# Optimization experiments

Hardware: AMD Instinct MI355X
Metric: run time of the kernel (lower is better)

Reference implementation:

```python
import jax, jax.numpy as jnp
import numpy as np

IN_DIM, HIDDEN_DIM, OUT_DIM = 128, 64, 64
N_NODES, N_EDGES = 100000, 1000000


def gcn_layer(x, src, dst, W, b):
    """PyG GCNConv: h = W x; out = D^-1/2 (A+I) D^-1/2 h + b (self-loops already in src/dst)."""
    n = x.shape[0]
    deg = jax.ops.segment_sum(jnp.ones_like(src, dtype=x.dtype), dst, num_segments=n)
    dinv = jnp.where(deg > 0, jax.lax.rsqrt(deg), 0.0)
    norm = dinv[src] * dinv[dst]          # [E+N]
    h = x @ W                              # [N, out]
    msg = h[src] * norm[:, None]           # [E+N, out] gather + scale
    out = jax.ops.segment_sum(msg, dst, num_segments=n)  # scatter-add
    return out + b


def setup_inputs() -> dict:
    key = jax.random.key(0)
    k1, k2, k3, k4 = jax.random.split(key, 4)
    x = jax.random.normal(k1, (N_NODES, IN_DIM), dtype=jnp.float32)
    edge_index = jax.random.randint(k2, (2, N_EDGES), 0, N_NODES, dtype=jnp.int64)
    # Glorot-ish init for the two GCNConv linear weights; zero biases (PyG default)
    W1 = jax.random.normal(k3, (IN_DIM, HIDDEN_DIM), dtype=jnp.float32) / np.sqrt(IN_DIM)
    W2 = jax.random.normal(k4, (HIDDEN_DIM, OUT_DIM), dtype=jnp.float32) / np.sqrt(HIDDEN_DIM)
    b1 = jnp.zeros((HIDDEN_DIM,), dtype=jnp.float32)
    b2 = jnp.zeros((OUT_DIM,), dtype=jnp.float32)
    return {"x": x, "edge_index": edge_index, "W1": W1, "b1": b1, "W2": W2, "b2": b2}


def reference(x, edge_index, W1, b1, W2, b2):
    n = x.shape[0]
    loops = jnp.arange(n, dtype=edge_index.dtype)
    src = jnp.concatenate([edge_index[0], loops])  # add self-loops once
    dst = jnp.concatenate([edge_index[1], loops])
    x1 = gcn_layer(x, src, dst, W1, b1)
    h = jax.nn.relu(x1)
    # dropout is identity in eval/reference mode
    x2 = gcn_layer(h, src, dst, W2, b2)
    return x2
```

## Files before the change

kernel.cpp:

```cpp
#include <hip/hip_runtime.h>
#include <hip/hip_fp16.h>

#define DIM_IN 128
#define DIM_HID 64
#define BK_SHIFT 9
#define BK_SIZE 512
#define SRC_BITS 17
#define CAP 6144
#define CAP2 8192
#define P_EPT  16
#define P_TILE 4096

typedef _Float16 half8 __attribute__((ext_vector_type(8)));
typedef float floatx4 __attribute__((ext_vector_type(4)));


__global__ void zero_kernel(int* __restrict__ bcur, float* __restrict__ dinv_sent) {
    bcur[threadIdx.x] = 0;
    if (threadIdx.x == 0) dinv_sent[0] = 0.0f;
}


__global__ __launch_bounds__(256)
void gemm1_partition_kernel(const float* __restrict__ x, const float* __restrict__ W,
                            _Float16* __restrict__ h, int n, int gb,
                            const int* __restrict__ src, const int* __restrict__ dst,
                            int* __restrict__ bcur, int* __restrict__ part, int E) {
    __shared__ int smem[5888];
    const int tid = threadIdx.x;

    if (blockIdx.x < gb) {
        constexpr int K = DIM_IN, LDK = K + 8;
        _Float16* Wt = (_Float16*)smem;
        for (int idx = tid; idx < K * 64; idx += 256) {
            int k = idx >> 6, c = idx & 63;
            Wt[c * LDK + k] = (_Float16)W[idx];
        }
        __syncthreads();

        const int wave = tid >> 6;
        const int lane = tid & 63;
        const int r    = lane & 15;
        const int g    = lane >> 4;
        const int row0 = blockIdx.x * 64 + wave * 16;
        const int arow = row0 + r;
        const float* xrow = x + (size_t)(arow < n ? arow : 0) * K + g * 8;

        floatx4 acc0 = {}, acc1 = {}, acc2 = {}, acc3 = {};
#pragma unroll
        for (int kt = 0; kt < K / 32; ++kt) {
            float4 a0 = *(const float4*)(xrow + kt * 32);
            float4 a1 = *(const float4*)(xrow + kt * 32 + 4);
            half8 a;
            a[0] = (_Float16)a0.x; a[1] = (_Float16)a0.y;
            a[2] = (_Float16)a0.z; a[3] = (_Float16)a0.w;
            a[4] = (_Float16)a1.x; a[5] = (_Float16)a1.y;
            a[6] = (_Float16)a1.z; a[7] = (_Float16)a1.w;

            const _Float16* wb = &Wt[r * LDK + kt * 32 + g * 8];
            half8 b0 = *(const half8*)(wb + 0 * 16 * LDK);
            half8 b1 = *(const half8*)(wb + 1 * 16 * LDK);
            half8 b2 = *(const half8*)(wb + 2 * 16 * LDK);
            half8 b3 = *(const half8*)(wb + 3 * 16 * LDK);
            acc0 = __builtin_amdgcn_mfma_f32_16x16x32_f16(a, b0, acc0, 0, 0, 0);
            acc1 = __builtin_amdgcn_mfma_f32_16x16x32_f16(a, b1, acc1, 0, 0, 0);
            acc2 = __builtin_amdgcn_mfma_f32_16x16x32_f16(a, b2, acc2, 0, 0, 0);
            acc3 = __builtin_amdgcn_mfma_f32_16x16x32_f16(a, b3, acc3, 0, 0, 0);
        }

#pragma unroll
        for (int j = 0; j < 4; ++j) {
            int drow = row0 + g * 4 + j;
            _Float16* o = h + (size_t)drow * 64 + r;
            if (drow < n) {
                o[0]  = (_Float16)acc0[j];
                o[16] = (_Float16)acc1[j];
                o[32] = (_Float16)acc2[j];
                o[48] = (_Float16)acc3[j];
            } else {
                o[0] = (_Float16)0; o[16] = (_Float16)0;
                o[32] = (_Float16)0; o[48] = (_Float16)0;
            }
        }
    } else {
        int* hist  = smem;
        int* bofs  = smem + 256;
        int* gbase = smem + 512;
        int* stage = smem + 768;
        unsigned char* auxb = (unsigned char*)(smem + 4864);
        const int tile0 = (blockIdx.x - gb) * P_TILE;
        const int tcnt  = min(P_TILE, E - tile0);

        hist[tid] = 0;
        __syncthreads();

        int pack[P_EPT], bb[P_EPT], lo[P_EPT];
#pragma unroll
        for (int i = 0; i < P_EPT; ++i) {
            int e = tile0 + i * 256 + tid;
            bb[i] = -1;
            if (e < E) {
                int d = dst[e];
                int s = src[e];
                bb[i]   = d >> BK_SHIFT;
                pack[i] = ((d & (BK_SIZE - 1)) << SRC_BITS) | s;
                lo[i]   = atomicAdd(&hist[bb[i]], 1);
            }
        }
        __syncthreads();

        bofs[tid] = hist[tid];
        __syncthreads();
        for (int off = 1; off < 256; off <<= 1) {
            int t = (tid >= off) ? bofs[tid - off] : 0;
            __syncthreads();
            bofs[tid] += t;
            __syncthreads();
        }
        int ex = bofs[tid] - hist[tid];
        __syncthreads();
        bofs[tid] = ex;
        if (hist[tid]) gbase[tid] = tid * CAP + atomicAdd(&bcur[tid], hist[tid]);
        __syncthreads();

#pragma unroll
        for (int i = 0; i < P_EPT; ++i) {
            if (bb[i] >= 0) {
                int p = bofs[bb[i]] + lo[i];
                stage[p] = pack[i];
                auxb[p]  = (unsigned char)bb[i];
            }
        }
        __syncthreads();

        for (int k = tid; k < tcnt; k += 256) {
            int b = auxb[k];
            part[gbase[b] + (k - bofs[b])] = stage[k];
        }
    }
}


__global__ __launch_bounds__(256)
void bucket_fill_kernel(const int* __restrict__ bcur, const int* __restrict__ part,
                        int2* __restrict__ nodeinfo, float* __restrict__ dinv,
                        int* __restrict__ srcs, int n, int zrow) {
    __shared__ int cnt[BK_SIZE];
    __shared__ int rp[BK_SIZE];
    __shared__ int s2[256];
    __shared__ int total;
    const int tid   = threadIdx.x;
    const int bid   = blockIdx.x;
    const int node0 = bid << BK_SHIFT;
    const int bs    = min(BK_SIZE, n - node0);
    const int pbase = bid * CAP;
    const int sbase = bid * CAP2;
    const int ecnt  = bcur[bid];

    cnt[tid] = 0; cnt[tid + 256] = 0;
    __syncthreads();
    for (int k = tid; k < ecnt; k += 256)
        atomicAdd(&cnt[part[pbase + k] >> SRC_BITS], 1);
    __syncthreads();

    int c0 = cnt[2 * tid], c1 = cnt[2 * tid + 1];
    int p0 = (c0 + 3) & ~3, p1 = (c1 + 3) & ~3;
    s2[tid] = p0 + p1;
    __syncthreads();
    for (int off = 1; off < 256; off <<= 1) {
        int t = (tid >= off) ? s2[tid - off] : 0;
        __syncthreads();
        s2[tid] += t;
        __syncthreads();
    }
    int ex = s2[tid] - (p0 + p1);
    rp[2 * tid]     = ex;
    rp[2 * tid + 1] = ex + p0;
    if (tid == 255) total = s2[255];
    __syncthreads();

    for (int i = tid; i < bs; i += 256) {
        int c = cnt[i];
        nodeinfo[node0 + i] = make_int2(sbase + rp[i], (c + 3) & ~3);
        dinv[node0 + i]     = rsqrtf((float)c + 1.0f);
    }
    __syncthreads();

    cnt[tid] = 0; cnt[tid + 256] = 0;
    __syncthreads();
    for (int k = tid; k < total; k += 256) srcs[sbase + k] = zrow;
    __syncthreads();
    for (int k = tid; k < ecnt; k += 256) {
        int v    = part[pbase + k];
        int li   = v >> SRC_BITS;
        int slot = atomicAdd(&cnt[li], 1);
        srcs[sbase + rp[li] + slot] = v & ((1 << SRC_BITS) - 1);
    }
}


__global__ __launch_bounds__(256)
void layer2_fused_kernel(const int2* __restrict__ nodeinfo, const int* __restrict__ srcs,
                         const float* __restrict__ dinv, const half8* __restrict__ hs,
                         const float* __restrict__ b1, const float* __restrict__ W2,
                         _Float16* __restrict__ h2, int n) {
    __shared__ _Float16 At[64 * 72];
    __shared__ _Float16 Wt[64 * 72];
    const int tid = threadIdx.x;

    for (int idx = tid; idx < 64 * 64; idx += 256) {
        int k = idx >> 6, c = idx & 63;
        Wt[c * 72 + k] = (_Float16)W2[idx];
    }

    const int f    = tid & 7;
    const int grp  = tid >> 3;
    const int row0 = blockIdx.x * 64;

#pragma unroll
    for (int rnd = 0; rnd < 2; ++rnd) {
        const int nrow = rnd * 32 + grp;
        const int node = row0 + nrow;
        half8 o = {};
        if (node < n) {
            int2 info = nodeinfo[node];
            int start = info.x, cpad = info.y;
            float dn = dinv[node];
            half8 sv = hs[(size_t)node * 8 + f];
            float acc[8];
#pragma unroll
            for (int i = 0; i < 8; ++i) acc[i] = dn * (float)sv[i];

            if (cpad > 0) {
                int4 ss = *(const int4*)&srcs[start];
                for (int j = 0; j < cpad; j += 4) {
                    int4 nxt = *(const int4*)&srcs[start + j + 4];
                    float d0 = dinv[ss.x], d1 = dinv[ss.y], d2 = dinv[ss.z], d3 = dinv[ss.w];
                    half8 v0 = hs[(size_t)ss.x * 8 + f];
                    half8 v1 = hs[(size_t)ss.y * 8 + f];
                    half8 v2 = hs[(size_t)ss.z * 8 + f];
                    half8 v3 = hs[(size_t)ss.w * 8 + f];
#pragma unroll
                    for (int i = 0; i < 8; ++i)
                        acc[i] += (d0 * (float)v0[i] + d1 * (float)v1[i]) +
                                  (d2 * (float)v2[i] + d3 * (float)v3[i]);
                    ss = nxt;
                }
            }
#pragma unroll
            for (int i = 0; i < 8; ++i) {
                float g1 = fmaf(acc[i], dn, b1[f * 8 + i]);
                o[i] = (_Float16)fmaxf(g1, 0.0f);
            }
        }
        *(half8*)&At[nrow * 72 + f * 8] = o;
    }
    __syncthreads();

    const int wave = tid >> 6;
    const int lane = tid & 63;
    const int r    = lane & 15;
    const int g    = lane >> 4;

    floatx4 acc0 = {}, acc1 = {}, acc2 = {}, acc3 = {};
#pragma unroll
    for (int kt = 0; kt < 2; ++kt) {
        half8 a = *(const half8*)&At[(wave * 16 + r) * 72 + kt * 32 + g * 8];
        const _Float16* wb = &Wt[r * 72 + kt * 32 + g * 8];
        half8 b0 = *(const half8*)(wb + 0 * 16 * 72);
        half8 b1v = *(const half8*)(wb + 1 * 16 * 72);
        half8 b2v = *(const half8*)(wb + 2 * 16 * 72);
        half8 b3v = *(const half8*)(wb + 3 * 16 * 72);
        acc0 = __builtin_amdgcn_mfma_f32_16x16x32_f16(a, b0, acc0, 0, 0, 0);
        acc1 = __builtin_amdgcn_mfma_f32_16x16x32_f16(a, b1v, acc1, 0, 0, 0);
        acc2 = __builtin_amdgcn_mfma_f32_16x16x32_f16(a, b2v, acc2, 0, 0, 0);
        acc3 = __builtin_amdgcn_mfma_f32_16x16x32_f16(a, b3v, acc3, 0, 0, 0);
    }

#pragma unroll
    for (int j = 0; j < 4; ++j) {
        int drow = row0 + wave * 16 + g * 4 + j;
        float dn2 = (drow < n) ? dinv[drow] : 0.0f;
        _Float16* o = h2 + (size_t)drow * 64 + r;
        o[0]  = (_Float16)(acc0[j] * dn2);
        o[16] = (_Float16)(acc1[j] * dn2);
        o[32] = (_Float16)(acc2[j] * dn2);
        o[48] = (_Float16)(acc3[j] * dn2);
    }
}


__global__ __launch_bounds__(256)
void gather_out_kernel(const int2* __restrict__ nodeinfo, const int* __restrict__ srcs,
                       const float* __restrict__ dinv, const half8* __restrict__ hs,
                       const float* __restrict__ b, float* __restrict__ out, int n) {
    const int tid  = threadIdx.x;
    const int f    = tid & 7;
    const int node = blockIdx.x * 32 + (tid >> 3);
    if (node >= n) return;

    int2 info = nodeinfo[node];
    int start = info.x, cpad = info.y;

    half8 sv = hs[(size_t)node * 8 + f];
    float acc[8];
#pragma unroll
    for (int i = 0; i < 8; ++i) acc[i] = (float)sv[i];

    if (cpad > 0) {
        int4 ss = *(const int4*)&srcs[start];
        for (int j = 0; j < cpad; j += 4) {
            int4 nxt = *(const int4*)&srcs[start + j + 4];
            half8 v0 = hs[(size_t)ss.x * 8 + f];
            half8 v1 = hs[(size_t)ss.y * 8 + f];
            half8 v2 = hs[(size_t)ss.z * 8 + f];
            half8 v3 = hs[(size_t)ss.w * 8 + f];
#pragma unroll
            for (int i = 0; i < 8; ++i)
                acc[i] += ((float)v0[i] + (float)v1[i]) + ((float)v2[i] + (float)v3[i]);
            ss = nxt;
        }
    }

    float dn = dinv[node];
    const float4* b4 = (const float4*)b;
    float4 bb0 = b4[f * 2], bb1 = b4[f * 2 + 1];
    float4 o0 = make_float4(fmaf(acc[0], dn, bb0.x), fmaf(acc[1], dn, bb0.y),
                            fmaf(acc[2], dn, bb0.z), fmaf(acc[3], dn, bb0.w));
    float4 o1 = make_float4(fmaf(acc[4], dn, bb1.x), fmaf(acc[5], dn, bb1.y),
                            fmaf(acc[6], dn, bb1.z), fmaf(acc[7], dn, bb1.w));
    float4* o4 = (float4*)out;
    o4[(size_t)node * 16 + f * 2]     = o0;
    o4[(size_t)node * 16 + f * 2 + 1] = o1;
}


extern "C" void kernel_launch(void* const* d_in, const int* in_sizes, int n_in,
                              void* d_out, int out_size, void* d_ws, size_t ws_size,
                              hipStream_t stream) {
    const float* x   = (const float*)d_in[0];
    const int*   ei  = (const int*)d_in[1];
    const float* W1  = (const float*)d_in[2];
    const float* b1  = (const float*)d_in[3];
    const float* W2  = (const float*)d_in[4];
    const float* b2  = (const float*)d_in[5];
    float*       out = (float*)d_out;

    const int n = in_sizes[0] / DIM_IN;
    const int E = in_sizes[1] / 2;
    const int* srcp = ei;
    const int* dstp = ei + E;
    const int NB    = (n + BK_SIZE - 1) >> BK_SHIFT;
    const int gb    = (n + 63) / 64;
    const int pb    = (E + P_TILE - 1) / P_TILE;
    const int ab    = (n + 31) / 32;
    const size_t nrows = (size_t)gb * 64;

    const int npad = ((n + 255) / 256) * 256;

    int*      bcur     = (int*)d_ws;
    int2*     nodeinfo = (int2*)(bcur + 256);
    float*    dinv     = (float*)((int*)nodeinfo + 2 * npad);
    int*      srcs     = (int*)(dinv + npad);
    int*      part     = srcs + (size_t)NB * CAP2;
    _Float16* h        = (_Float16*)(part + (size_t)NB * CAP);
    _Float16* h2       = h + nrows * 64;

    zero_kernel<<<1, 256, 0, stream>>>(bcur, &dinv[n]);
    gemm1_partition_kernel<<<gb + pb, 256, 0, stream>>>(x, W1, h, n, gb,
                                                        srcp, dstp, bcur, part, E);
    bucket_fill_kernel<<<NB, 256, 0, stream>>>(bcur, part, nodeinfo, dinv, srcs, n, n);
    layer2_fused_kernel<<<gb, 256, 0, stream>>>(nodeinfo, srcs, dinv, (const half8*)h,
                                                b1, W2, h2, n);
    gather_out_kernel<<<ab, 256, 0, stream>>>(nodeinfo, srcs, dinv, (const half8*)h2,
                                              b2, out, n);
}
```

Baseline: 102.1 us.

## Co-schedule GEMM1 with bucket fill instead of partition, halve partition tile

Moves the layer-1 GEMM out of the partition launch and into the bucket-fill launch, so the GEMM blocks run alongside the few (~196) bucket-fill blocks instead of alongside the many partition blocks. This is meant to fill otherwise idle CUs during bucket fill. The partition tile shrinks from 4096 to 2048 edges per block, giving more blocks and less shared memory per block. The full-region zero-row fill is replaced by padding only each node's tail slots, cutting redundant stores.

```diff
diff --git a/kernel.cpp b/kernel.cpp
--- a/kernel.cpp
+++ b/kernel.cpp
@@ -8,8 +8,8 @@
 #define SRC_BITS 17
 #define CAP 6144
 #define CAP2 8192
-#define P_EPT  16
-#define P_TILE 4096
+#define P_EPT  8
+#define P_TILE 2048
 
 typedef _Float16 half8 __attribute__((ext_vector_type(8)));
 typedef float floatx4 __attribute__((ext_vector_type(4)));
@@ -22,14 +22,129 @@
 
 
 __global__ __launch_bounds__(256)
-void gemm1_partition_kernel(const float* __restrict__ x, const float* __restrict__ W,
-                            _Float16* __restrict__ h, int n, int gb,
-                            const int* __restrict__ src, const int* __restrict__ dst,
-                            int* __restrict__ bcur, int* __restrict__ part, int E) {
-    __shared__ int smem[5888];
+void partition_kernel(const int* __restrict__ src, const int* __restrict__ dst,
+                      int* __restrict__ bcur, int* __restrict__ part, int E) {
+    __shared__ int hist[256];
+    __shared__ int bofs[256];
+    __shared__ int gbase[256];
+    __shared__ int stage[P_TILE];
+    __shared__ unsigned char auxb[P_TILE];
+    const int tid   = threadIdx.x;
+    const int tile0 = blockIdx.x * P_TILE;
+    const int tcnt  = min(P_TILE, E - tile0);
+
+    hist[tid] = 0;
+    __syncthreads();
+
+    int pack[P_EPT], bb[P_EPT], lo[P_EPT];
+#pragma unroll
+    for (int i = 0; i < P_EPT; ++i) {
+        int e = tile0 + i * 256 + tid;
+        bb[i] = -1;
+        if (e < E) {
+            int d = dst[e];
+            int s = src[e];
+            bb[i]   = d >> BK_SHIFT;
+            pack[i] = ((d & (BK_SIZE - 1)) << SRC_BITS) | s;
+            lo[i]   = atomicAdd(&hist[bb[i]], 1);
+        }
+    }
+    __syncthreads();
+
+    bofs[tid] = hist[tid];
+    __syncthreads();
+    for (int off = 1; off < 256; off <<= 1) {
+        int t = (tid >= off) ? bofs[tid - off] : 0;
+        __syncthreads();
+        bofs[tid] += t;
+        __syncthreads();
+    }
+    int ex = bofs[tid] - hist[tid];
+    __syncthreads();
+    bofs[tid] = ex;
+    if (hist[tid]) gbase[tid] = tid * CAP + atomicAdd(&bcur[tid], hist[tid]);
+    __syncthreads();
+
+#pragma unroll
+    for (int i = 0; i < P_EPT; ++i) {
+        if (bb[i] >= 0) {
+            int p = bofs[bb[i]] + lo[i];
+            stage[p] = pack[i];
+            auxb[p]  = (unsigned char)bb[i];
+        }
+    }
+    __syncthreads();
+
+    for (int k = tid; k < tcnt; k += 256) {
+        int b = auxb[k];
+        part[gbase[b] + (k - bofs[b])] = stage[k];
+    }
+}
+
+
+__global__ __launch_bounds__(256)
+void fill_gemm1_kernel(const int* __restrict__ bcur, const int* __restrict__ part,
+                       int2* __restrict__ nodeinfo, float* __restrict__ dinv,
+                       int* __restrict__ srcs, int n, int NB,
+                       const float* __restrict__ x, const float* __restrict__ W,
+                       _Float16* __restrict__ h) {
+    __shared__ int smem[4352];
     const int tid = threadIdx.x;
 
-    if (blockIdx.x < gb) {
+    if (blockIdx.x < (unsigned)NB) {
+        int* cnt = smem;
+        int* rp  = smem + 512;
+        int* s2  = smem + 1024;
+        const int bid   = blockIdx.x;
+        const int node0 = bid << BK_SHIFT;
+        const int bs    = min(BK_SIZE, n - node0);
+        const int pbase = bid * CAP;
+        const int sbase = bid * CAP2;
+        const int ecnt  = bcur[bid];
+
+        cnt[tid] = 0; cnt[tid + 256] = 0;
+        __syncthreads();
+        for (int k = tid; k < ecnt; k += 256)
+            atomicAdd(&cnt[part[pbase + k] >> SRC_BITS], 1);
+        __syncthreads();
+
+        int c0 = cnt[2 * tid], c1 = cnt[2 * tid + 1];
+        int p0 = (c0 + 3) & ~3, p1 = (c1 + 3) & ~3;
+        s2[tid] = p0 + p1;
+        __syncthreads();
+        for (int off = 1; off < 256; off <<= 1) {
+            int t = (tid >= off) ? s2[tid - off] : 0;
+            __syncthreads();
+            s2[tid] += t;
+            __syncthreads();
+        }
+        int ex = s2[tid] - (p0 + p1);
+        rp[2 * tid]     = ex;
+        rp[2 * tid + 1] = ex + p0;
+        __syncthreads();
+
+        for (int i = tid; i < bs; i += 256) {
+            int c = cnt[i];
+            nodeinfo[node0 + i] = make_int2(sbase + rp[i], (c + 3) & ~3);
+            dinv[node0 + i]     = rsqrtf((float)c + 1.0f);
+        }
+        __syncthreads();
+
+        cnt[tid] = 0; cnt[tid + 256] = 0;
+        __syncthreads();
+        for (int k = tid; k < ecnt; k += 256) {
+            int v    = part[pbase + k];
+            int li   = v >> SRC_BITS;
+            int slot = atomicAdd(&cnt[li], 1);
+            srcs[sbase + rp[li] + slot] = v & ((1 << SRC_BITS) - 1);
+        }
+        __syncthreads();
+        for (int i = tid; i < bs; i += 256) {
+            int c = cnt[i];
+            int cp = (c + 3) & ~3;
+            for (int k = c; k < cp; ++k) srcs[sbase + rp[i] + k] = n;
+        }
+    } else {
         constexpr int K = DIM_IN, LDK = K + 8;
         _Float16* Wt = (_Float16*)smem;
         for (int idx = tid; idx < K * 64; idx += 256) {
@@ -42,7 +157,7 @@
         const int lane = tid & 63;
         const int r    = lane & 15;
         const int g    = lane >> 4;
-        const int row0 = blockIdx.x * 64 + wave * 16;
+        const int row0 = (blockIdx.x - NB) * 64 + wave * 16;
         const int arow = row0 + r;
         const float* xrow = x + (size_t)(arow < n ? arow : 0) * K + g * 8;
 
@@ -82,119 +197,6 @@
                 o[32] = (_Float16)0; o[48] = (_Float16)0;
             }
         }
-    } else {
-        int* hist  = smem;
-        int* bofs  = smem + 256;
-        int* gbase = smem + 512;
-        int* stage = smem + 768;
-        unsigned char* auxb = (unsigned char*)(smem + 4864);
-        const int tile0 = (blockIdx.x - gb) * P_TILE;
-        const int tcnt  = min(P_TILE, E - tile0);
-
-        hist[tid] = 0;
-        __syncthreads();
-
-        int pack[P_EPT], bb[P_EPT], lo[P_EPT];
-#pragma unroll
-        for (int i = 0; i < P_EPT; ++i) {
-            int e = tile0 + i * 256 + tid;
-            bb[i] = -1;
-            if (e < E) {
-                int d = dst[e];
-                int s = src[e];
-                bb[i]   = d >> BK_SHIFT;
-                pack[i] = ((d & (BK_SIZE - 1)) << SRC_BITS) | s;
-                lo[i]   = atomicAdd(&hist[bb[i]], 1);
-            }
-        }
-        __syncthreads();
-
-        bofs[tid] = hist[tid];
-        __syncthreads();
-        for (int off = 1; off < 256; off <<= 1) {
-            int t = (tid >= off) ? bofs[tid - off] : 0;
-            __syncthreads();
-            bofs[tid] += t;
-            __syncthreads();
-        }
-        int ex = bofs[tid] - hist[tid];
-        __syncthreads();
-        bofs[tid] = ex;
-        if (hist[tid]) gbase[tid] = tid * CAP + atomicAdd(&bcur[tid], hist[tid]);
-        __syncthreads();
-
-#pragma unroll
-        for (int i = 0; i < P_EPT; ++i) {
-            if (bb[i] >= 0) {
-                int p = bofs[bb[i]] + lo[i];
-                stage[p] = pack[i];
-                auxb[p]  = (unsigned char)bb[i];
-            }
-        }
-        __syncthreads();
-
-        for (int k = tid; k < tcnt; k += 256) {
-            int b = auxb[k];
-            part[gbase[b] + (k - bofs[b])] = stage[k];
-        }
-    }
-}
-
-
-__global__ __launch_bounds__(256)
-void bucket_fill_kernel(const int* __restrict__ bcur, const int* __restrict__ part,
-                        int2* __restrict__ nodeinfo, float* __restrict__ dinv,
-                        int* __restrict__ srcs, int n, int zrow) {
-    __shared__ int cnt[BK_SIZE];
-    __shared__ int rp[BK_SIZE];
-    __shared__ int s2[256];
-    __shared__ int total;
-    const int tid   = threadIdx.x;
-    const int bid   = blockIdx.x;
-    const int node0 = bid << BK_SHIFT;
-    const int bs    = min(BK_SIZE, n - node0);
-    const int pbase = bid * CAP;
-    const int sbase = bid * CAP2;
-    const int ecnt  = bcur[bid];
-
-    cnt[tid] = 0; cnt[tid + 256] = 0;
-    __syncthreads();
-    for (int k = tid; k < ecnt; k += 256)
-        atomicAdd(&cnt[part[pbase + k] >> SRC_BITS], 1);
-    __syncthreads();
-
-    int c0 = cnt[2 * tid], c1 = cnt[2 * tid + 1];
-    int p0 = (c0 + 3) & ~3, p1 = (c1 + 3) & ~3;
-    s2[tid] = p0 + p1;
-    __syncthreads();
-    for (int off = 1; off < 256; off <<= 1) {
-        int t = (tid >= off) ? s2[tid - off] : 0;
-        __syncthreads();
-        s2[tid] += t;
-        __syncthreads();
-    }
-    int ex = s2[tid] - (p0 + p1);
-    rp[2 * tid]     = ex;
-    rp[2 * tid + 1] = ex + p0;
-    if (tid == 255) total = s2[255];
-    __syncthreads();
-
-    for (int i = tid; i < bs; i += 256) {
-        int c = cnt[i];
-        nodeinfo[node0 + i] = make_int2(sbase + rp[i], (c + 3) & ~3);
-        dinv[node0 + i]     = rsqrtf((float)c + 1.0f);
-    }
-    __syncthreads();
-
-    cnt[tid] = 0; cnt[tid + 256] = 0;
-    __syncthreads();
-    for (int k = tid; k < total; k += 256) srcs[sbase + k] = zrow;
-    __syncthreads();
-    for (int k = tid; k < ecnt; k += 256) {
-        int v    = part[pbase + k];
-        int li   = v >> SRC_BITS;
-        int slot = atomicAdd(&cnt[li], 1);
-        srcs[sbase + rp[li] + slot] = v & ((1 << SRC_BITS) - 1);
     }
 }
 
@@ -367,9 +369,9 @@
     _Float16* h2       = h + nrows * 64;
 
     zero_kernel<<<1, 256, 0, stream>>>(bcur, &dinv[n]);
-    gemm1_partition_kernel<<<gb + pb, 256, 0, stream>>>(x, W1, h, n, gb,
-                                                        srcp, dstp, bcur, part, E);
-    bucket_fill_kernel<<<NB, 256, 0, stream>>>(bcur, part, nodeinfo, dinv, srcs, n, n);
+    partition_kernel<<<pb, 256, 0, stream>>>(srcp, dstp, bcur, part, E);
+    fill_gemm1_kernel<<<NB + gb, 256, 0, stream>>>(bcur, part, nodeinfo, dinv, srcs, n, NB,
+                                                   x, W1, h);
     layer2_fused_kernel<<<gb, 256, 0, stream>>>(nodeinfo, srcs, dinv, (const half8*)h,
                                                 b1, W2, h2, n);
     gather_out_kernel<<<ab, 256, 0, stream>>>(nodeinfo, srcs, dinv, (const half8*)h2,
```

Result: no change. 102.3 us (+0.2%).
